# Performance work log

Hardware: AMD Instinct MI355X
Metric: run time of the kernel (lower is better)

## Reference

```python
import jax, jax.numpy as jnp
import numpy as np

L, N, K, F, H = 6, 32768, 8, 32, 256  # levels, nodes/level, fan-in, feat_dim, hidden_dim


def setup_inputs() -> dict:
    key = jax.random.key(0)
    ks = jax.random.split(key, 10)
    sc = lambda k, shape, fan: (jax.random.normal(k, shape, jnp.float32) / np.sqrt(fan).astype(np.float32))
    return {
        "feats": jax.random.normal(ks[0], (L, N, F), jnp.float32),
        "pred_idx": jax.random.randint(ks[1], (L - 1, N, K), 0, N),
        "We": sc(ks[2], (H, F), F),
        "be": jnp.zeros((H,), jnp.float32),
        "rs_W1": sc(ks[3], (12, H, H), H),
        "rs_b1": jnp.zeros((12, H), jnp.float32),
        "rs_W2": sc(ks[4], (12, H, H), H),
        "rs_b2": jnp.zeros((12, H), jnp.float32),
        "rs_W3": sc(ks[5], (12, H, H), H),
        "rs_b3": jnp.zeros((12, H), jnp.float32),
        "rc_W1": sc(ks[6], (6, 2 * H, 2 * H), 2 * H),
        "rc_b1": jnp.zeros((6, 2 * H), jnp.float32),
        "rc_W2": sc(ks[7], (6, 2 * H, 2 * H), 2 * H),
        "rc_b2": jnp.zeros((6, 2 * H), jnp.float32),
        "rc_W3": sc(ks[8], (6, H, 2 * H), 2 * H),
        "rc_b3": jnp.zeros((6, H), jnp.float32),
    }


def _resnet(W1, b1, W2, b2, W3, b3, x):
    # lay3(tanh(lay2(tanh(lay1(x)))) + x)
    h1 = jnp.tanh(x @ W1.T + b1)
    h2 = jnp.tanh(h1 @ W2.T + b2)
    return (h2 + x) @ W3.T + b3


def reference(feats, pred_idx, We, be,
              rs_W1, rs_b1, rs_W2, rs_b2, rs_W3, rs_b3,
              rc_W1, rc_b1, rc_W2, rc_b2, rc_W3, rc_b3):
    # rs (h,h,h) order: [d1_mp, d1_mp1, d2_mp, d2_mp1, d3_mp, d3_mp1,
    #                    d1_node1, d2_node1, d3_node1, d1_comb1, d2_comb1, d3_comb1]
    # rc (2h,2h,h) order: [d1_node, d2_node, d3_node, d1_comb, d2_comb, d3_comb]
    small = lambda i, x: _resnet(rs_W1[i], rs_b1[i], rs_W2[i], rs_b2[i], rs_W3[i], rs_b3[i], x)
    big = lambda i, x: _resnet(rc_W1[i], rc_b1[i], rc_W2[i], rc_b2[i], rc_W3[i], rc_b3[i], x)

    n_levels = feats.shape[0]
    embeds = []
    for l in range(n_levels):  # sequential topological dependency (fixed, small L)
        e = jnp.tanh(feats[l] @ We.T + be)  # embed_op
        if l > 0:
            d = min(l - 1, 2)  # bwd_depth -> d1/d2/d3 branch
            # comb_embed branch: 'bwd_node_embeds' field exists but is DGL's
            # zero-initialized default for this frontier -> concat with zeros.
            x = jnp.concatenate([e, jnp.zeros_like(e)], axis=-1)
            e = jnp.tanh(small(9 + d, jnp.tanh(big(3 + d, x))))
            # message: gather predecessor embeds, sum-reduce, mp resnets
            msgs = jnp.sum(embeds[l - 1][pred_idx[l - 1]], axis=1)  # [N, H]
            r = jnp.tanh(small(2 * d, msgs))
            r = jnp.tanh(small(2 * d + 1, r))
            # node_embeds branch: concat(embeds, msgs_redux)
            x2 = jnp.concatenate([e, r], axis=-1)
            e = jnp.tanh(small(6 + d, jnp.tanh(big(d, x2))))
        embeds.append(e)
    return jnp.stack(embeds)  # graph.ndata['bwd_node_embeds'], [L, N, H]
```

## Files before the change

kernel.cpp:

```cpp
#include <hip/hip_runtime.h>

#define NLVL 6
#define NN   32768
#define KFAN 8
#define FDIM 32
#define HDIM 256

typedef __attribute__((ext_vector_type(4))) float f32x4;
typedef __attribute__((ext_vector_type(8))) _Float16 f16x8;
typedef __attribute__((ext_vector_type(4))) unsigned short u16x4;

__device__ __forceinline__ float h2f(unsigned short u) {
    _Float16 h; __builtin_memcpy(&h, &u, 2); return (float)h;
}
__device__ __forceinline__ unsigned short f2h(float f) {
    _Float16 h = (_Float16)f;
    unsigned short u; __builtin_memcpy(&u, &h, 2); return u;
}
__device__ __forceinline__ float tanh_fast(float x) {
    float e = __expf(2.0f * x);
    return 1.0f - 2.0f / (e + 1.0f);
}
__device__ __forceinline__ void gload16(const void* g, void* l) {
    __builtin_amdgcn_global_load_lds((const __attribute__((address_space(1))) void*)g,
                                     (__attribute__((address_space(3))) void*)l, 16, 0, 0);
}

template<int KLEN, int ROWB, int MFR>
__device__ __forceinline__ void layer_mm(const unsigned short* sA,
                                         const unsigned short* __restrict__ Wg, int ldw,
                                         int rbase, int wcol, int lane,
                                         f32x4 (&acc)[MFR][4])
{
    const int fr = lane & 15, fq = lane >> 4;
    #pragma unroll
    for (int m = 0; m < MFR; ++m)
        #pragma unroll
        for (int n = 0; n < 4; ++n)
            acc[m][n] = (f32x4){0.f, 0.f, 0.f, 0.f};

    constexpr int NKS = KLEN / 32;
    f16x8 avA[MFR], avB[MFR], bvA[4], bvB[4];

    auto ldB = [&](int ks, f16x8* bv) {
        #pragma unroll
        for (int n = 0; n < 4; ++n)
            bv[n] = *(const f16x8*)(Wg + (size_t)(wcol + n * 16 + fr) * ldw + ks * 32 + fq * 8);
    };
    auto ldA = [&](int ks, f16x8* av) {
        #pragma unroll
        for (int m = 0; m < MFR; ++m) {
            const int rr = rbase + m * 16 + fr;
            const int byt = rr * ROWB + ((ks * 64 + fq * 16) ^ ((rr & 7) << 4));
            av[m] = *(const f16x8*)((const char*)sA + byt);
        }
    };
    auto mm = [&](f16x8* av, f16x8* bv) {
        #pragma unroll
        for (int m = 0; m < MFR; ++m)
            #pragma unroll
            for (int n = 0; n < 4; ++n)
                acc[m][n] = __builtin_amdgcn_mfma_f32_16x16x32_f16(av[m], bv[n], acc[m][n], 0, 0, 0);
    };

    ldA(0, avA); ldB(0, bvA);
    #pragma unroll
    for (int s = 0; s < NKS / 2; ++s) {
        ldA(2 * s + 1, avB); ldB(2 * s + 1, bvB);
        mm(avA, bvA);
        if (2 * s + 2 < NKS) { ldA(2 * s + 2, avA); ldB(2 * s + 2, bvA); }
        mm(avB, bvB);
    }
}

template<int BM, int KD, int K1, bool GATHER, bool F32OUT>
__global__ __launch_bounds__(512, 2)
void resnet_fused(const unsigned short* __restrict__ X, int ldx,
                  const int* __restrict__ gidx,
                  const unsigned short* __restrict__ gsrc,
                  const unsigned short* __restrict__ W1, const float* __restrict__ b1,
                  const unsigned short* __restrict__ W2, const float* __restrict__ b2,
                  const unsigned short* __restrict__ W3, const float* __restrict__ b3,
                  unsigned short* __restrict__ outB, int ldo,
                  float* __restrict__ outF)
{
    __shared__ __align__(16) unsigned short sX[BM * K1];
    __shared__ __align__(16) unsigned short sH[BM * KD];
    constexpr int ROWBX = K1 * 2, ROWBH = KD * 2;

    const int tid = threadIdx.x, lane = tid & 63, wid = tid >> 6;
    const int brow = blockIdx.x * BM;
    const int fr = lane & 15, fq = lane >> 4;

    if (GATHER) {
        constexpr int CB = K1 / 8;
        for (int i = tid; i < BM * CB; i += 512) {
            const int row = i / CB, cb = i % CB;
            const int* ip = gidx + (size_t)(brow + row) * KFAN;
            float s[8] = {0.f, 0.f, 0.f, 0.f, 0.f, 0.f, 0.f, 0.f};
            #pragma unroll
            for (int k = 0; k < KFAN; ++k) {
                f16x8 v = *(const f16x8*)(gsrc + (size_t)ip[k] * HDIM + cb * 8);
                #pragma unroll
                for (int j = 0; j < 8; ++j) s[j] += (float)v[j];
            }
            f16x8 o;
            #pragma unroll
            for (int j = 0; j < 8; ++j) o[j] = (_Float16)s[j];
            *(f16x8*)((char*)sX + row * ROWBX + ((cb * 16) ^ ((row & 7) << 4))) = o;
        }
    } else {
        constexpr int ROUNDS = BM * K1 * 2 / (512 * 16);
        #pragma unroll
        for (int r = 0; r < ROUNDS; ++r) {
            const int lin = (r * 512 + tid) * 16;
            const int row = lin / ROWBX;
            const int cb  = (lin % ROWBX) >> 4;
            const int scb = cb ^ (row & 7);
            gload16(X + (size_t)(brow + row) * ldx + scb * 8,
                    (char*)sX + (lin - lane * 16));
        }
    }
    __syncthreads();

    constexpr int NWC12 = KD / 64;
    const int wc12 = (wid % NWC12) * 64;
    const int rb12 = (wid / NWC12) * 64;
    {
        f32x4 a1[4][4];
        layer_mm<K1, ROWBX, 4>(sX, W1, KD, rb12, wc12, lane, a1);
        #pragma unroll
        for (int m = 0; m < 4; ++m)
            #pragma unroll
            for (int n = 0; n < 4; ++n) {
                const int col = wc12 + n * 16 + fr;
                const float bb = b1[col];
                #pragma unroll
                for (int j = 0; j < 4; ++j) {
                    const int row = rb12 + m * 16 + fq * 4 + j;
                    const float v = tanh_fast(a1[m][n][j] + bb);
                    *(unsigned short*)((char*)sH + row * ROWBH + ((col * 2) ^ ((row & 7) << 4))) = f2h(v);
                }
            }
    }
    __syncthreads();

    {
        f32x4 a2[4][4];
        layer_mm<KD, ROWBH, 4>(sH, W2, KD, rb12, wc12, lane, a2);
        #pragma unroll
        for (int m = 0; m < 4; ++m)
            #pragma unroll
            for (int n = 0; n < 4; ++n) {
                const int col = wc12 + n * 16 + fr;
                const float bb = b2[col];
                #pragma unroll
                for (int j = 0; j < 4; ++j) {
                    const int row = rb12 + m * 16 + fq * 4 + j;
                    float v = tanh_fast(a2[m][n][j] + bb);
                    if (col < K1)
                        v += h2f(*(const unsigned short*)((const char*)sX + row * ROWBX + ((col * 2) ^ ((row & 7) << 4))));
                    a2[m][n][j] = v;
                }
            }
        __syncthreads();
        #pragma unroll
        for (int m = 0; m < 4; ++m)
            #pragma unroll
            for (int n = 0; n < 4; ++n) {
                const int col = wc12 + n * 16 + fr;
                #pragma unroll
                for (int j = 0; j < 4; ++j) {
                    const int row = rb12 + m * 16 + fq * 4 + j;
                    *(unsigned short*)((char*)sH + row * ROWBH + ((col * 2) ^ ((row & 7) << 4))) = f2h(a2[m][n][j]);
                }
            }
    }
    __syncthreads();

    {
        constexpr int WM3 = BM / 2, MFR3 = WM3 / 16;
        const int wc3 = (wid & 3) * 64;
        const int rb3 = (wid >> 2) * WM3;
        f32x4 a3[MFR3][4];
        layer_mm<KD, ROWBH, MFR3>(sH, W3, KD, rb3, wc3, lane, a3);
        #pragma unroll
        for (int m = 0; m < MFR3; ++m)
            #pragma unroll
            for (int n = 0; n < 4; ++n) {
                const int col = wc3 + n * 16 + fr;
                const float bb = b3[col];
                #pragma unroll
                for (int j = 0; j < 4; ++j) {
                    const int row = rb3 + m * 16 + fq * 4 + j;
                    const float v = tanh_fast(a3[m][n][j] + bb);
                    const size_t gr = (size_t)(brow + row);
                    outB[gr * ldo + col] = f2h(v);
                    if (F32OUT) outF[gr * HDIM + col] = v;
                }
            }
    }
}

template<bool F32OUT>
__global__ __launch_bounds__(256)
void embed_kernel(const float* __restrict__ feats,
                  const float* __restrict__ We,
                  const float* __restrict__ be,
                  unsigned short* __restrict__ outB, int ldo,
                  float* __restrict__ outF)
{
    __shared__ float sW[256 * 33];
    __shared__ float sF[16 * 32];
    const int t = threadIdx.x;
    #pragma unroll
    for (int i = 0; i < 32; ++i) {
        int idx = t + 256 * i;
        sW[(idx >> 5) * 33 + (idx & 31)] = We[idx];
    }
    const size_t base = (size_t)blockIdx.x * 16;
    for (int i = t; i < 16 * 32; i += 256) sF[i] = feats[base * 32 + i];
    __syncthreads();

    const float bb = be[t];
    for (int r = 0; r < 16; ++r) {
        float a = bb;
        #pragma unroll
        for (int k = 0; k < 32; ++k) a += sF[r * 32 + k] * sW[t * 33 + k];
        const float v = tanh_fast(a);
        const size_t row = base + r;
        outB[row * ldo + t] = f2h(v);
        if (F32OUT) outF[row * HDIM + t] = v;
    }
}

__global__ __launch_bounds__(256)
void cvt_kernel(const float* __restrict__ in, unsigned short* __restrict__ out, int n4)
{
    const int i = blockIdx.x * 256 + threadIdx.x;
    if (i >= n4) return;
    const float4 v = ((const float4*)in)[i];
    u16x4 o;
    o[0] = f2h(v.x); o[1] = f2h(v.y); o[2] = f2h(v.z); o[3] = f2h(v.w);
    ((u16x4*)out)[i] = o;
}

extern "C" void kernel_launch(void* const* d_in, const int* in_sizes, int n_in,
                              void* d_out, int out_size, void* d_ws, size_t ws_size,
                              hipStream_t stream)
{
    const float* feats    = (const float*)d_in[0];
    const int*   pred_idx = (const int*)d_in[1];
    const float* We       = (const float*)d_in[2];
    const float* be       = (const float*)d_in[3];
    const float* rs_W1    = (const float*)d_in[4];
    const float* rs_b1    = (const float*)d_in[5];
    const float* rs_W2    = (const float*)d_in[6];
    const float* rs_b2    = (const float*)d_in[7];
    const float* rs_W3    = (const float*)d_in[8];
    const float* rs_b3    = (const float*)d_in[9];
    const float* rc_W1    = (const float*)d_in[10];
    const float* rc_b1    = (const float*)d_in[11];
    const float* rc_W2    = (const float*)d_in[12];
    const float* rc_b2    = (const float*)d_in[13];
    const float* rc_W3    = (const float*)d_in[14];
    const float* rc_b3    = (const float*)d_in[15];
    float* out = (float*)d_out;

    char* ws = (char*)d_ws;
    size_t off = 0;
    auto alloc = [&](size_t bytes) -> unsigned short* {
        unsigned short* p = (unsigned short*)(ws + off);
        off += (bytes + 255) & ~(size_t)255;
        return p;
    };
    unsigned short* rcW1b = alloc((size_t)6 * 512 * 512 * 2);
    unsigned short* rcW2b = alloc((size_t)6 * 512 * 512 * 2);
    unsigned short* rcW3b = alloc((size_t)6 * 256 * 512 * 2);
    unsigned short* rsW1b = alloc((size_t)12 * 256 * 256 * 2);
    unsigned short* rsW2b = alloc((size_t)12 * 256 * 256 * 2);
    unsigned short* rsW3b = alloc((size_t)12 * 256 * 256 * 2);
    unsigned short* xcat  = alloc((size_t)NN * 256 * 2);
    unsigned short* p0    = alloc((size_t)NN * 512 * 2);
    unsigned short* Tb    = alloc((size_t)NN * 256 * 2);
    unsigned short* q0    = alloc((size_t)NN * 256 * 2);
    unsigned short* ebfA  = alloc((size_t)NN * 256 * 2);
    unsigned short* ebfB  = alloc((size_t)NN * 256 * 2);
    (void)ws_size; (void)in_sizes; (void)n_in; (void)out_size;

    auto cvt = [&](const float* src, unsigned short* dst, int n) {
        int n4 = n / 4;
        cvt_kernel<<<dim3((n4 + 255) / 256), dim3(256), 0, stream>>>(src, dst, n4);
    };
    cvt(rc_W1, rcW1b, 6 * 512 * 512);
    cvt(rc_W2, rcW2b, 6 * 512 * 512);
    cvt(rc_W3, rcW3b, 6 * 256 * 512);
    cvt(rs_W1, rsW1b, 12 * 256 * 256);
    cvt(rs_W2, rsW2b, 12 * 256 * 256);
    cvt(rs_W3, rsW3b, 12 * 256 * 256);

    auto smallRN = [&](int i, const unsigned short* x, int ldx,
                       unsigned short* ob, int ldo, float* of,
                       const int* gidx, const unsigned short* gsrc) {
        const unsigned short* w1 = rsW1b + (size_t)i * 256 * 256;
        const unsigned short* w2 = rsW2b + (size_t)i * 256 * 256;
        const unsigned short* w3 = rsW3b + (size_t)i * 256 * 256;
        const float* B1 = rs_b1 + i * 256;
        const float* B2 = rs_b2 + i * 256;
        const float* B3 = rs_b3 + i * 256;
        if (gidx)
            resnet_fused<128, 256, 256, true, false><<<dim3(NN / 128), dim3(512), 0, stream>>>(
                nullptr, 0, gidx, gsrc, w1, B1, w2, B2, w3, B3, ob, ldo, nullptr);
        else if (of)
            resnet_fused<128, 256, 256, false, true><<<dim3(NN / 128), dim3(512), 0, stream>>>(
                x, ldx, nullptr, nullptr, w1, B1, w2, B2, w3, B3, ob, ldo, of);
        else
            resnet_fused<128, 256, 256, false, false><<<dim3(NN / 128), dim3(512), 0, stream>>>(
                x, ldx, nullptr, nullptr, w1, B1, w2, B2, w3, B3, ob, ldo, nullptr);
    };
    auto bigRN = [&](int i, bool halfK, const unsigned short* x, int ldx, unsigned short* ob) {
        const unsigned short* w1 = rcW1b + (size_t)i * 512 * 512;
        const unsigned short* w2 = rcW2b + (size_t)i * 512 * 512;
        const unsigned short* w3 = rcW3b + (size_t)i * 256 * 512;
        const float* B1 = rc_b1 + i * 512;
        const float* B2 = rc_b2 + i * 512;
        const float* B3 = rc_b3 + i * 256;
        if (halfK)
            resnet_fused<64, 512, 256, false, false><<<dim3(NN / 64), dim3(512), 0, stream>>>(
                x, ldx, nullptr, nullptr, w1, B1, w2, B2, w3, B3, ob, 256, nullptr);
        else
            resnet_fused<64, 512, 512, false, false><<<dim3(NN / 64), dim3(512), 0, stream>>>(
                x, ldx, nullptr, nullptr, w1, B1, w2, B2, w3, B3, ob, 256, nullptr);
    };

    unsigned short* ebp = ebfA;
    unsigned short* ebc = ebfB;

    embed_kernel<true><<<dim3(NN / 16), dim3(256), 0, stream>>>(
        feats, We, be, ebp, 256, out);

    for (int l = 1; l < NLVL; ++l) {
        const int d = (l - 1 < 2) ? (l - 1) : 2;
        const float* fl = feats + (size_t)l * NN * FDIM;
        const int* idx_l = pred_idx + (size_t)(l - 1) * NN * KFAN;

        embed_kernel<false><<<dim3(NN / 16), dim3(256), 0, stream>>>(
            fl, We, be, xcat, 256, nullptr);

        bigRN(3 + d, true, xcat, 256, Tb);
        smallRN(9 + d, Tb, 256, p0, 512, nullptr, nullptr, nullptr);

        smallRN(2 * d,     nullptr, 0, q0, 256, nullptr, idx_l, ebp);
        smallRN(2 * d + 1, q0, 256, p0 + 256, 512, nullptr, nullptr, nullptr);

        bigRN(d, false, p0, 512, Tb);
        smallRN(6 + d, Tb, 256, ebc, 256, out + (size_t)l * NN * HDIM, nullptr, nullptr);

        unsigned short* tmp = ebp; ebp = ebc; ebc = tmp;
    }
}
```

Measured before the change: 2.159 ms.

## Halve row tiles and raise occupancy target in fused resnet kernel

Halves the rows each block handles in the fused resnet kernels (128→64 for the small resnets, 64→32 for the big ones) and makes the per-warp row fragments of the first two layers depend on the tile size. Launch bounds go from 2 to 4 blocks per CU, and the leading dimension of the weight matrix becomes a compile-time constant. The K loop becomes a single double-buffered loop, and the gather loop is unrolled. Smaller tiles and more resident blocks are meant to hide latency better, at the cost of re-reading the weights from global memory more often and possible register pressure or spills under the tighter bound.

```diff
diff --git a/kernel.cpp b/kernel.cpp
--- a/kernel.cpp
+++ b/kernel.cpp
@@ -26,9 +26,9 @@
                                      (__attribute__((address_space(3))) void*)l, 16, 0, 0);
 }
 
-template<int KLEN, int ROWB, int MFR>
+template<int KLEN, int ROWB, int MFR, int LDW>
 __device__ __forceinline__ void layer_mm(const unsigned short* sA,
-                                         const unsigned short* __restrict__ Wg, int ldw,
+                                         const unsigned short* __restrict__ Wg,
                                          int rbase, int wcol, int lane,
                                          f32x4 (&acc)[MFR][4])
 {
@@ -40,41 +40,37 @@
             acc[m][n] = (f32x4){0.f, 0.f, 0.f, 0.f};
 
     constexpr int NKS = KLEN / 32;
-    f16x8 avA[MFR], avB[MFR], bvA[4], bvB[4];
-
-    auto ldB = [&](int ks, f16x8* bv) {
+    f16x8 av[2][MFR], bv[2][4];
+    const unsigned short* Wbase = Wg + (size_t)(wcol + fr) * LDW + fq * 8;
+
+    auto ldB = [&](int ks, int buf) {
         #pragma unroll
         for (int n = 0; n < 4; ++n)
-            bv[n] = *(const f16x8*)(Wg + (size_t)(wcol + n * 16 + fr) * ldw + ks * 32 + fq * 8);
-    };
-    auto ldA = [&](int ks, f16x8* av) {
+            bv[buf][n] = *(const f16x8*)(Wbase + n * 16 * LDW + ks * 32);
+    };
+    auto ldA = [&](int ks, int buf) {
         #pragma unroll
         for (int m = 0; m < MFR; ++m) {
             const int rr = rbase + m * 16 + fr;
             const int byt = rr * ROWB + ((ks * 64 + fq * 16) ^ ((rr & 7) << 4));
-            av[m] = *(const f16x8*)((const char*)sA + byt);
+            av[buf][m] = *(const f16x8*)((const char*)sA + byt);
         }
     };
-    auto mm = [&](f16x8* av, f16x8* bv) {
+
+    ldA(0, 0); ldB(0, 0);
+    #pragma unroll
+    for (int s = 0; s < NKS; ++s) {
+        if (s + 1 < NKS) { ldA(s + 1, (s + 1) & 1); ldB(s + 1, (s + 1) & 1); }
         #pragma unroll
         for (int m = 0; m < MFR; ++m)
             #pragma unroll
             for (int n = 0; n < 4; ++n)
-                acc[m][n] = __builtin_amdgcn_mfma_f32_16x16x32_f16(av[m], bv[n], acc[m][n], 0, 0, 0);
-    };
-
-    ldA(0, avA); ldB(0, bvA);
-    #pragma unroll
-    for (int s = 0; s < NKS / 2; ++s) {
-        ldA(2 * s + 1, avB); ldB(2 * s + 1, bvB);
-        mm(avA, bvA);
-        if (2 * s + 2 < NKS) { ldA(2 * s + 2, avA); ldB(2 * s + 2, bvA); }
-        mm(avB, bvB);
+                acc[m][n] = __builtin_amdgcn_mfma_f32_16x16x32_f16(av[s & 1][m], bv[s & 1][n], acc[m][n], 0, 0, 0);
     }
 }
 
 template<int BM, int KD, int K1, bool GATHER, bool F32OUT>
-__global__ __launch_bounds__(512, 2)
+__global__ __launch_bounds__(512, 4)
 void resnet_fused(const unsigned short* __restrict__ X, int ldx,
                   const int* __restrict__ gidx,
                   const unsigned short* __restrict__ gsrc,
@@ -94,7 +90,9 @@
 
     if (GATHER) {
         constexpr int CB = K1 / 8;
-        for (int i = tid; i < BM * CB; i += 512) {
+        #pragma unroll
+        for (int r = 0; r < BM * CB / 512; ++r) {
+            const int i = r * 512 + tid;
             const int row = i / CB, cb = i % CB;
             const int* ip = gidx + (size_t)(brow + row) * KFAN;
             float s[8] = {0.f, 0.f, 0.f, 0.f, 0.f, 0.f, 0.f, 0.f};
@@ -124,13 +122,17 @@
     __syncthreads();
 
     constexpr int NWC12 = KD / 64;
+    constexpr int NWR12 = 8 / NWC12;
+    constexpr int RPG12 = BM / NWR12;
+    constexpr int MFR12 = RPG12 / 16;
     const int wc12 = (wid % NWC12) * 64;
-    const int rb12 = (wid / NWC12) * 64;
+    const int rb12 = (wid / NWC12) * RPG12;
+
     {
-        f32x4 a1[4][4];
-        layer_mm<K1, ROWBX, 4>(sX, W1, KD, rb12, wc12, lane, a1);
-        #pragma unroll
-        for (int m = 0; m < 4; ++m)
+        f32x4 a1[MFR12][4];
+        layer_mm<K1, ROWBX, MFR12, KD>(sX, W1, rb12, wc12, lane, a1);
+        #pragma unroll
+        for (int m = 0; m < MFR12; ++m)
             #pragma unroll
             for (int n = 0; n < 4; ++n) {
                 const int col = wc12 + n * 16 + fr;
@@ -146,10 +148,10 @@
     __syncthreads();
 
     {
-        f32x4 a2[4][4];
-        layer_mm<KD, ROWBH, 4>(sH, W2, KD, rb12, wc12, lane, a2);
-        #pragma unroll
-        for (int m = 0; m < 4; ++m)
+        f32x4 a2[MFR12][4];
+        layer_mm<KD, ROWBH, MFR12, KD>(sH, W2, rb12, wc12, lane, a2);
+        #pragma unroll
+        for (int m = 0; m < MFR12; ++m)
             #pragma unroll
             for (int n = 0; n < 4; ++n) {
                 const int col = wc12 + n * 16 + fr;
@@ -165,7 +167,7 @@
             }
         __syncthreads();
         #pragma unroll
-        for (int m = 0; m < 4; ++m)
+        for (int m = 0; m < MFR12; ++m)
             #pragma unroll
             for (int n = 0; n < 4; ++n) {
                 const int col = wc12 + n * 16 + fr;
@@ -179,11 +181,12 @@
     __syncthreads();
 
     {
-        constexpr int WM3 = BM / 2, MFR3 = WM3 / 16;
+        constexpr int RPG3 = BM / 2;
+        constexpr int MFR3 = RPG3 / 16;
         const int wc3 = (wid & 3) * 64;
-        const int rb3 = (wid >> 2) * WM3;
+        const int rb3 = (wid >> 2) * RPG3;
         f32x4 a3[MFR3][4];
-        layer_mm<KD, ROWBH, MFR3>(sH, W3, KD, rb3, wc3, lane, a3);
+        layer_mm<KD, ROWBH, MFR3, KD>(sH, W3, rb3, wc3, lane, a3);
         #pragma unroll
         for (int m = 0; m < MFR3; ++m)
             #pragma unroll
@@ -309,13 +312,13 @@
         const float* B2 = rs_b2 + i * 256;
         const float* B3 = rs_b3 + i * 256;
         if (gidx)
-            resnet_fused<128, 256, 256, true, false><<<dim3(NN / 128), dim3(512), 0, stream>>>(
+            resnet_fused<64, 256, 256, true, false><<<dim3(NN / 64), dim3(512), 0, stream>>>(
                 nullptr, 0, gidx, gsrc, w1, B1, w2, B2, w3, B3, ob, ldo, nullptr);
         else if (of)
-            resnet_fused<128, 256, 256, false, true><<<dim3(NN / 128), dim3(512), 0, stream>>>(
+            resnet_fused<64, 256, 256, false, true><<<dim3(NN / 64), dim3(512), 0, stream>>>(
                 x, ldx, nullptr, nullptr, w1, B1, w2, B2, w3, B3, ob, ldo, of);
         else
-            resnet_fused<128, 256, 256, false, false><<<dim3(NN / 128), dim3(512), 0, stream>>>(
+            resnet_fused<64, 256, 256, false, false><<<dim3(NN / 64), dim3(512), 0, stream>>>(
                 x, ldx, nullptr, nullptr, w1, B1, w2, B2, w3, B3, ob, ldo, nullptr);
     };
     auto bigRN = [&](int i, bool halfK, const unsigned short* x, int ldx, unsigned short* ob) {
@@ -326,10 +329,10 @@
         const float* B2 = rc_b2 + i * 512;
         const float* B3 = rc_b3 + i * 256;
         if (halfK)
-            resnet_fused<64, 512, 256, false, false><<<dim3(NN / 64), dim3(512), 0, stream>>>(
+            resnet_fused<32, 512, 256, false, false><<<dim3(NN / 32), dim3(512), 0, stream>>>(
                 x, ldx, nullptr, nullptr, w1, B1, w2, B2, w3, B3, ob, 256, nullptr);
         else
-            resnet_fused<64, 512, 512, false, false><<<dim3(NN / 64), dim3(512), 0, stream>>>(
+            resnet_fused<32, 512, 512, false, false><<<dim3(NN / 32), dim3(512), 0, stream>>>(
                 x, ldx, nullptr, nullptr, w1, B1, w2, B2, w3, B3, ob, 256, nullptr);
     };
 
```

Measured after the change: 3.016 ms. 39.7% more time.
